# Kernel tuning notes

Measured on AMD Instinct MI355X. Metric: run time of the kernel, lower is better.

The kernel has to match this reference:

```python
import jax, jax.numpy as jnp
import numpy as np

FILTERS = 64
NBITS = 4
NUE = 4
NSPU = 2
NST = NUE * NSPU           # 8 streams total
OUT_CH = NST * NBITS       # 32 output channels
NBS, NANT = 1, 16
CIN = NBS * NANT * 2 + NBS * NANT * NUE * NSPU * 2 + NUE * NSPU + 1  # 297


def hard_sigmoid(x):
    # Keras ConvLSTM2D default recurrent_activation
    return jnp.clip(0.2 * x + 0.5, 0.0, 1.0)


def conv2d(x, w):
    # x: [N,H,W,C], w: [kh,kw,Cin,Cout], SAME padding
    return jax.lax.conv_general_dilated(x, w, (1, 1), 'SAME',
                                        dimension_numbers=('NHWC', 'HWIO', 'NHWC'))


def convlstm2d(x, Wx, Wh, b):
    """Keras ConvLSTM2D (return_sequences=True), gate order i,f,c,o.
    x: [B,T,H,W,Cin] -> [B,T,H,W,F].
    Input-to-hidden convs are precomputed for all timesteps at once;
    only the cheap hidden-to-hidden conv is inside the scan."""
    B, T, H, W, Cin = x.shape
    F = Wh.shape[2]
    xz = conv2d(x.reshape(B * T, H, W, Cin), Wx).reshape(B, T, H, W, 4 * F) + b
    xz = jnp.moveaxis(xz, 1, 0)  # [T,B,H,W,4F]
    h0 = jnp.zeros((B, H, W, F), x.dtype)

    def step(carry, z_in):
        h, c = carry
        z = z_in + conv2d(h, Wh)
        zi, zf, zg, zo = jnp.split(z, 4, axis=-1)
        i = hard_sigmoid(zi)
        f = hard_sigmoid(zf)
        g = jnp.tanh(zg)
        o = hard_sigmoid(zo)
        c = f * c + i * g
        h = o * jnp.tanh(c)
        return (h, c), h

    _, hs = jax.lax.scan(step, (h0, h0), xz)
    return jnp.moveaxis(hs, 0, 1)  # [B,T,H,W,F]


def _lstm_params(key, cin, f, scale=0.05):
    k1, k2, k3 = jax.random.split(key, 3)
    Wx = jax.random.normal(k1, (3, 3, cin, 4 * f), jnp.float32) * scale
    Wh = jax.random.normal(k2, (3, 3, f, 4 * f), jnp.float32) * scale
    b = jax.random.normal(k3, (4 * f,), jnp.float32) * scale
    return Wx, Wh, b


def setup_inputs() -> dict:
    key = jax.random.key(0)
    ks = jax.random.split(key, 10)
    B, T, W = 2, 14, 1536
    inp = {
        'y_ri': jax.random.normal(ks[0], (B, NBS, NANT, T, W, 2), jnp.float32),
        'h_ri': jax.random.normal(ks[1], (B, NBS, NANT, NUE, NSPU, T, W, 2), jnp.float32),
        'err_var': jax.random.uniform(ks[2], (1, 1, 1, NUE, NSPU, T, W), jnp.float32),
        'no': jax.random.uniform(ks[3], (1,), jnp.float32),
    }
    inp['Wx_in'], inp['Wh_in'], inp['b_in'] = _lstm_params(ks[4], CIN, FILTERS)
    inp['Wx_r0'], inp['Wh_r0'], inp['b_r0'] = _lstm_params(ks[5], FILTERS, FILTERS)
    inp['Wx_r1'], inp['Wh_r1'], inp['b_r1'] = _lstm_params(ks[6], FILTERS, FILTERS)
    inp['Wx_out'], inp['Wh_out'], inp['b_out'] = _lstm_params(ks[7], FILTERS, OUT_CH)
    return inp


def _forward(y_ri, h_ri, err_var, no,
             Wx_in, Wh_in, b_in,
             Wx_r0, Wh_r0, b_r0,
             Wx_r1, Wh_r1, b_r1,
             Wx_out, Wh_out, b_out):
    B, nbs, nant, T, W, _ = y_ri.shape
    # y: [B,nbs,nant,T,W,2] -> [B,T,W,nbs*nant*2]
    y_feats = jnp.transpose(y_ri, (0, 3, 4, 1, 2, 5)).reshape(B, T, W, -1)
    # h: [B,nbs,nant,ue,spu,T,W,2] -> [B,T,W,nbs*nant*ue*spu*2]
    h_feats = jnp.transpose(h_ri, (0, 5, 6, 1, 2, 3, 4, 7)).reshape(B, T, W, -1)
    # err_var: [1,1,1,ue,spu,T,W] -> [B,T,W,ue*spu]
    ev = jnp.transpose(err_var[0, 0, 0], (2, 3, 0, 1)).reshape(1, T, W, NUE * NSPU)
    err_feats = jnp.broadcast_to(ev, (B, T, W, NUE * NSPU))
    no_feat = jnp.broadcast_to(no.reshape(1, 1, 1, 1), (B, T, W, 1))
    z = jnp.concatenate([y_feats, h_feats, err_feats, no_feat], axis=-1)
    z = z[:, :, :, None, :]  # [B,T,W,1,C]

    z = convlstm2d(z, Wx_in, Wh_in, b_in)
    # residual blocks (in_ch == filters, so identity skip)
    z = convlstm2d(z, Wx_r0, Wh_r0, b_r0) + z
    z = convlstm2d(z, Wx_r1, Wh_r1, b_r1) + z
    z = convlstm2d(z, Wx_out, Wh_out, b_out)

    z = z[:, :, :, 0, :]  # [B,T,W,OUT_CH]
    N = T * W
    z = z.reshape(B, N, NUE, NSPU, NBITS)
    z = jnp.transpose(z, (0, 2, 3, 1, 4))
    return z.reshape(B, NUE, NSPU, N * NBITS)


def reference(y_ri, h_ri, err_var, no,
              Wx_in, Wh_in, b_in,
              Wx_r0, Wh_r0, b_r0,
              Wx_r1, Wh_r1, b_r1,
              Wx_out, Wh_out, b_out):
    return _forward(y_ri, h_ri, err_var, no,
                    Wx_in, Wh_in, b_in,
                    Wx_r0, Wh_r0, b_r0,
                    Wx_r1, Wh_r1, b_r1,
                    Wx_out, Wh_out, b_out)
```

## Files before the change

### kernel.cpp

```cpp
#include <hip/hip_runtime.h>
#include <hip/hip_bf16.h>


#define BB   2
#define TT   14
#define LL   1536
#define LL2  1538
#define CINR 297
#define CP_IN 320
#define NSTRIP 96
#define NBLK  (BB * NSTRIP)
#define WIN  48

typedef __attribute__((ext_vector_type(8))) short short8;
typedef __attribute__((ext_vector_type(4))) float floatx4;

static constexpr size_t U_WBIN_HI  = 0;
static constexpr size_t U_WBIN_LO  = 245760;
static constexpr size_t U_WBR0_HI  = 491520;
static constexpr size_t U_WBR0_LO  = 540672;
static constexpr size_t U_WBR1_HI  = 589824;
static constexpr size_t U_WBR1_LO  = 638976;
static constexpr size_t U_WBOUT_HI = 688128;
static constexpr size_t U_WBOUT_LO = 712704;
static constexpr size_t U_WHTIN    = 737280;
static constexpr size_t U_WHTR0    = 786432;
static constexpr size_t U_WHTR1    = 835584;
static constexpr size_t U_WHTOUT   = 884736;
static constexpr size_t OFF_BIN   = 448512;
static constexpr size_t OFF_BR0   = 448768;
static constexpr size_t OFF_BR1   = 449024;
static constexpr size_t OFF_BOUT  = 449280;
static constexpr size_t OFF_Z0HI  = 458752;
static constexpr size_t SZ_Z0PL   = 6890240;
static constexpr size_t OFF_Z0LO  = OFF_Z0HI + SZ_Z0PL;
static constexpr size_t OFF_XZ    = OFF_Z0LO + SZ_Z0PL;
static constexpr size_t SZ_XZ     = (size_t)BB*TT*LL*256;
static constexpr size_t OFF_SEQ   = OFF_Z0HI;
static constexpr size_t OFF_SEQHI = OFF_SEQ + (size_t)BB*TT*LL2*64;
static constexpr size_t OFF_SEQLO = OFF_SEQHI + (size_t)BB*TT*LL2*32;

__device__ __forceinline__ float hsig(float x) {
    return fminf(fmaxf(0.2f * x + 0.5f, 0.0f), 1.0f);
}
__device__ __forceinline__ float ftanh(float x) {
    float e = __expf(2.0f * x);
    return 1.0f - 2.0f / (e + 1.0f);
}
__device__ __forceinline__ unsigned short f2bf(float x) {
    unsigned int u = __builtin_bit_cast(unsigned int, x);
    u += 0x7fffu + ((u >> 16) & 1u);
    return (unsigned short)(u >> 16);
}
__device__ __forceinline__ float bf2f(unsigned short h) {
    unsigned int u = ((unsigned int)h) << 16;
    return __builtin_bit_cast(float, u);
}

__global__ __launch_bounds__(256)
void zero_pads_kernel(unsigned short* __restrict__ z0hi,
                      unsigned short* __restrict__ z0lo)
{
    int idx = blockIdx.x * 256 + threadIdx.x;
    const int NZ = BB * TT * 2 * CP_IN;
    if (idx < NZ) {
        int c = idx % CP_IN, r2 = idx / CP_IN;
        int p = r2 >> 1, e = r2 & 1;
        long long off = ((long long)p * LL2 + (e ? (LL2 - 1) : 0)) * CP_IN + c;
        z0hi[off] = 0; z0lo[off] = 0;
    }
}

__global__ __launch_bounds__(256)
void zero_seq_pads_kernel(unsigned short* __restrict__ seqhb,
                          unsigned short* __restrict__ seqlb)
{
    int idx = blockIdx.x * 256 + threadIdx.x;
    const int NS = BB * TT * 2 * 64;
    if (idx < NS) {
        int c = idx % 64, r2 = idx / 64;
        int p = r2 >> 1, e = r2 & 1;
        long long off = ((long long)p * LL2 + (e ? (LL2 - 1) : 0)) * 64 + c;
        seqhb[off] = 0; seqlb[off] = 0;
    }
}

__global__ __launch_bounds__(256)
void prep_weights_kernel(const float* wx_in, const float* wh_in, const float* b_in,
                         const float* wx_r0, const float* wh_r0, const float* b_r0,
                         const float* wx_r1, const float* wh_r1, const float* b_r1,
                         const float* wx_out, const float* wh_out, const float* b_out,
                         float* __restrict__ ws)
{
    int idx = blockIdx.x * 256 + threadIdx.x;
    unsigned short* u = (unsigned short*)ws;
    if (idx < 245760) {
        int j = idx & 7, lane = (idx >> 3) & 63, frag = idx >> 9;
        int g = frag & 15, rest = frag >> 4;
        int kh = rest % 3, cc = rest / 3;
        int mm = lane & 15, quad = lane >> 4;
        int n = g * 16 + mm;
        int ci = cc * 32 + quad * 8 + j;
        float v = 0.0f;
        if (ci < CINR)
            v = wx_in[((size_t)(kh * 3 + 1) * CINR + ci) * 256 + (n & 3) * 64 + (n >> 2)];
        unsigned short hi = f2bf(v);
        u[U_WBIN_HI + idx] = hi;
        u[U_WBIN_LO + idx] = f2bf(v - bf2f(hi));
        return;
    }
    idx -= 245760;
    if (idx < 49152) {
        int j = idx & 7, lane = (idx >> 3) & 63, frag = idx >> 9;
        int g = frag & 15, rest = frag >> 4;
        int kh = rest % 3, cc = rest / 3;
        int mm = lane & 15, quad = lane >> 4;
        int n = g * 16 + mm;
        int ci = cc * 32 + quad * 8 + j;
        float v = wx_r0[((size_t)(kh * 3 + 1) * 64 + ci) * 256 + (n & 3) * 64 + (n >> 2)];
        unsigned short hi = f2bf(v);
        u[U_WBR0_HI + idx] = hi;
        u[U_WBR0_LO + idx] = f2bf(v - bf2f(hi));
        return;
    }
    idx -= 49152;
    if (idx < 49152) {
        int j = idx & 7, lane = (idx >> 3) & 63, frag = idx >> 9;
        int g = frag & 15, rest = frag >> 4;
        int kh = rest % 3, cc = rest / 3;
        int mm = lane & 15, quad = lane >> 4;
        int n = g * 16 + mm;
        int ci = cc * 32 + quad * 8 + j;
        float v = wx_r1[((size_t)(kh * 3 + 1) * 64 + ci) * 256 + (n & 3) * 64 + (n >> 2)];
        unsigned short hi = f2bf(v);
        u[U_WBR1_HI + idx] = hi;
        u[U_WBR1_LO + idx] = f2bf(v - bf2f(hi));
        return;
    }
    idx -= 49152;
    if (idx < 24576) {
        int j = idx & 7, lane = (idx >> 3) & 63, frag = idx >> 9;
        int g = frag & 7, rest = frag >> 3;
        int kh = rest % 3, cc = rest / 3;
        int mm = lane & 15, quad = lane >> 4;
        int n = g * 16 + mm;
        int ci = cc * 32 + quad * 8 + j;
        float v = wx_out[((size_t)(kh * 3 + 1) * 64 + ci) * 128 + (n & 3) * 32 + (n >> 2)];
        unsigned short hi = f2bf(v);
        u[U_WBOUT_HI + idx] = hi;
        u[U_WBOUT_LO + idx] = f2bf(v - bf2f(hi));
        return;
    }
    idx -= 24576;
    if (idx < 49152) {
        int n = idx / 192, k = idx % 192, kh = k >> 6, ci = k & 63;
        u[U_WHTIN + idx] = f2bf(wh_in[((size_t)(kh * 3 + 1) * 64 + ci) * 256 + n]);
        return;
    }
    idx -= 49152;
    if (idx < 49152) {
        int n = idx / 192, k = idx % 192, kh = k >> 6, ci = k & 63;
        u[U_WHTR0 + idx] = f2bf(wh_r0[((size_t)(kh * 3 + 1) * 64 + ci) * 256 + n]);
        return;
    }
    idx -= 49152;
    if (idx < 49152) {
        int n = idx / 192, k = idx % 192, kh = k >> 6, ci = k & 63;
        u[U_WHTR1 + idx] = f2bf(wh_r1[((size_t)(kh * 3 + 1) * 64 + ci) * 256 + n]);
        return;
    }
    idx -= 49152;
    if (idx < 12288) {
        int n = idx / 96, k = idx % 96, kh = k / 32, ci = k % 32;
        u[U_WHTOUT + idx] = f2bf(wh_out[((size_t)(kh * 3 + 1) * 32 + ci) * 128 + n]);
        return;
    }
    idx -= 12288;
    if (idx < 256) { int f = idx >> 2, g = idx & 3; ws[OFF_BIN + idx] = b_in[g * 64 + f]; return; }
    idx -= 256;
    if (idx < 256) { int f = idx >> 2, g = idx & 3; ws[OFF_BR0 + idx] = b_r0[g * 64 + f]; return; }
    idx -= 256;
    if (idx < 256) { int f = idx >> 2, g = idx & 3; ws[OFF_BR1 + idx] = b_r1[g * 64 + f]; return; }
    idx -= 256;
    if (idx < 128) { int f = idx >> 2, g = idx & 3; ws[OFF_BOUT + idx] = b_out[g * 32 + f]; return; }
}

__global__ __launch_bounds__(256)
void build_features_kernel(const float* __restrict__ y,
                           const float* __restrict__ h,
                           const float* __restrict__ ev,
                           const float* __restrict__ no,
                           unsigned short* __restrict__ z0hi,
                           unsigned short* __restrict__ z0lo)
{
    long long idx = (long long)blockIdx.x * 256 + threadIdx.x;
    const long long total = (long long)BB * TT * LL * CP_IN;
    if (idx >= total) return;
    int c = (int)(idx % CP_IN);
    long long rest = idx / CP_IN;
    int l = (int)(rest % LL); rest /= LL;
    int t = (int)(rest % TT);
    int b = (int)(rest / TT);
    float v = 0.0f;
    if (c < 32) {
        int na = c >> 1, ri = c & 1;
        v = y[((((long long)b * 16 + na) * TT + t) * LL + l) * 2 + ri];
    } else if (c < 288) {
        int q = c - 32;
        int ri = q & 1, nspu = (q >> 1) & 1, nue = (q >> 2) & 3, na = q >> 4;
        v = h[((((((long long)b * 16 + na) * 4 + nue) * 2 + nspu) * TT + t) * LL + l) * 2 + ri];
    } else if (c < 296) {
        int q = c - 288; int nspu = q & 1, nue = q >> 1;
        v = ev[(((long long)(nue * 2 + nspu) * TT + t) * LL) + l];
    } else if (c == 296) {
        v = no[0];
    }
    const long long widx = (((long long)(b * TT + t)) * LL2 + (l + 1)) * CP_IN + c;
    unsigned short hi = f2bf(v);
    z0hi[widx] = hi;
    z0lo[widx] = f2bf(v - bf2f(hi));
}

template <int CP>
__global__ __launch_bounds__(256)
void xz_gemm_mfma_kernel(const unsigned short* __restrict__ Ahi,
                         const unsigned short* __restrict__ Alo,
                         const unsigned short* __restrict__ Bphi,
                         const unsigned short* __restrict__ Bplo,
                         const float* __restrict__ bias,
                         float* __restrict__ out, int Ncol)
{
    constexpr int NCm = CP / 64;
    __shared__ unsigned short AsHi[66 * 72], AsLo[66 * 72];
    const int tid  = threadIdx.x;
    const int lane = tid & 63;
    const int wv   = tid >> 6;
    const int m    = lane & 15;
    const int quad = lane >> 4;
    const int bt   = blockIdx.y;
    const int l0   = blockIdx.x * 64;
    const int n0   = blockIdx.z * 128;
    const int NG   = Ncol >> 4;
    const int gBase = (n0 >> 4) + wv;

    const int r0s = tid >> 3,        c0 = (tid & 7) * 8;
    const int r1s = (tid + 256) >> 3, c1 = (tid & 7) * 8;
    const int r2s = 64 + (tid >> 3),  c2 = (tid & 7) * 8;
    const long long aG0 = ((long long)bt * LL2 + l0 + r0s) * CP + c0;
    const long long aG1 = ((long long)bt * LL2 + l0 + r1s) * CP + c1;
    const long long aG2 = ((long long)bt * LL2 + l0 + r2s) * CP + c2;

    short8 g0h, g0l, g1h, g1l, g2h = (short8)0, g2l = (short8)0;

    g0h = *reinterpret_cast<const short8*>(&Ahi[aG0]);
    g0l = *reinterpret_cast<const short8*>(&Alo[aG0]);
    g1h = *reinterpret_cast<const short8*>(&Ahi[aG1]);
    g1l = *reinterpret_cast<const short8*>(&Alo[aG1]);
    if (tid < 16) {
        g2h = *reinterpret_cast<const short8*>(&Ahi[aG2]);
        g2l = *reinterpret_cast<const short8*>(&Alo[aG2]);
    }

    floatx4 acc[4][2];
#pragma unroll
    for (int i = 0; i < 4; i++)
#pragma unroll
        for (int j = 0; j < 2; j++) acc[i][j] = (floatx4){0.f, 0.f, 0.f, 0.f};

#pragma unroll 1
    for (int mc = 0; mc < NCm; ++mc) {
        __syncthreads();
        *reinterpret_cast<short8*>(&AsHi[r0s * 72 + c0]) = g0h;
        *reinterpret_cast<short8*>(&AsLo[r0s * 72 + c0]) = g0l;
        *reinterpret_cast<short8*>(&AsHi[r1s * 72 + c1]) = g1h;
        *reinterpret_cast<short8*>(&AsLo[r1s * 72 + c1]) = g1l;
        if (tid < 16) {
            *reinterpret_cast<short8*>(&AsHi[r2s * 72 + c2]) = g2h;
            *reinterpret_cast<short8*>(&AsLo[r2s * 72 + c2]) = g2l;
        }
        __syncthreads();
        if (mc + 1 < NCm) {
            const int co = (mc + 1) * 64;
            g0h = *reinterpret_cast<const short8*>(&Ahi[aG0 + co]);
            g0l = *reinterpret_cast<const short8*>(&Alo[aG0 + co]);
            g1h = *reinterpret_cast<const short8*>(&Ahi[aG1 + co]);
            g1l = *reinterpret_cast<const short8*>(&Alo[aG1 + co]);
            if (tid < 16) {
                g2h = *reinterpret_cast<const short8*>(&Ahi[aG2 + co]);
                g2l = *reinterpret_cast<const short8*>(&Alo[aG2 + co]);
            }
        }
#pragma unroll
        for (int sub = 0; sub < 2; ++sub) {
            const int cc = mc * 2 + sub;
            short8 bh[3][2], bl[3][2];
#pragma unroll
            for (int kh = 0; kh < 3; ++kh)
#pragma unroll
                for (int nt = 0; nt < 2; ++nt) {
                    const size_t off =
                        ((size_t)((cc * 3 + kh) * NG + gBase + nt * 4)) * 512 + lane * 8;
                    bh[kh][nt] = *reinterpret_cast<const short8*>(&Bphi[off]);
                    bl[kh][nt] = *reinterpret_cast<const short8*>(&Bplo[off]);
                }
#pragma unroll
            for (int kh = 0; kh < 3; ++kh) {
#pragma unroll
                for (int mt = 0; mt < 4; ++mt) {
                    const int aofs = (mt * 16 + m + kh) * 72 + sub * 32 + quad * 8;
                    const short8 ah = *reinterpret_cast<const short8*>(&AsHi[aofs]);
                    const short8 al = *reinterpret_cast<const short8*>(&AsLo[aofs]);
                    acc[mt][0] = __builtin_amdgcn_mfma_f32_16x16x32_bf16(al, bh[kh][0], acc[mt][0], 0, 0, 0);
                    acc[mt][0] = __builtin_amdgcn_mfma_f32_16x16x32_bf16(ah, bl[kh][0], acc[mt][0], 0, 0, 0);
                    acc[mt][0] = __builtin_amdgcn_mfma_f32_16x16x32_bf16(ah, bh[kh][0], acc[mt][0], 0, 0, 0);
                    acc[mt][1] = __builtin_amdgcn_mfma_f32_16x16x32_bf16(al, bh[kh][1], acc[mt][1], 0, 0, 0);
                    acc[mt][1] = __builtin_amdgcn_mfma_f32_16x16x32_bf16(ah, bl[kh][1], acc[mt][1], 0, 0, 0);
                    acc[mt][1] = __builtin_amdgcn_mfma_f32_16x16x32_bf16(ah, bh[kh][1], acc[mt][1], 0, 0, 0);
                }
            }
        }
    }

#pragma unroll
    for (int nt = 0; nt < 2; ++nt) {
        const int col = n0 + nt * 64 + wv * 16 + m;
        const float bv = bias[col];
#pragma unroll
        for (int mt = 0; mt < 4; ++mt) {
#pragma unroll
            for (int reg = 0; reg < 4; ++reg) {
                int l = l0 + mt * 16 + quad * 4 + reg;
                out[((size_t)bt * LL + l) * Ncol + col] = acc[mt][nt][reg] + bv;
            }
        }
    }
}

template <int F_, bool RESID, bool OUTW>
__global__ __launch_bounds__(64 * (F_ / 16))
void lstm_scan_kernel(const float* __restrict__ xz,
                      const unsigned short* __restrict__ WhT,
                      float* seq,
                      unsigned short* __restrict__ seqhb,
                      unsigned short* __restrict__ seqlb,
                      float* __restrict__ dout)
{
    constexpr int NW = F_ / 16;
    constexpr int NT = 64 * NW;
    constexpr int K  = 3 * F_;
    constexpr int KS = K / 32;
    constexpr int KH = KS / 3;
    constexpr int HP = F_ + 8;
    __shared__ unsigned short Hs[2][(WIN + 2) * HP];

    const int tid  = threadIdx.x;
    const int lane = tid & 63;
    const int wv   = tid >> 6;
    const int m    = lane & 15;
    const int quad = lane >> 4;
    const int blk  = blockIdx.x;
    const int b    = blk / NSTRIP;
    const int o0   = (blk % NSTRIP) * 16;
    const int f    = wv * 16 + m;

    short8 bfr[4][KS];
#pragma unroll
    for (int g = 0; g < 4; g++)
#pragma unroll
        for (int ks = 0; ks < KS; ks++) {
            const int n  = g * F_ + f;
            const int k0 = ks * 32 + quad * 8;
            bfr[g][ks] = *reinterpret_cast<const short8*>(&WhT[(size_t)n * K + k0]);
        }

    for (int idx = tid; idx < (WIN + 2) * HP; idx += NT) {
        Hs[0][idx] = 0; Hs[1][idx] = 0;
    }
    __syncthreads();

    float c[3][4];
#pragma unroll
    for (int i = 0; i < 3; i++)
#pragma unroll
        for (int j = 0; j < 4; j++) c[i][j] = 0.0f;

    int cur = 0;
    for (int t = 0; t < TT; ++t) {
        const size_t btL  = ((size_t)b * TT + t) * LL;
        const size_t btLP = ((size_t)b * TT + t) * LL2;

        float4 xzv[3][4];
        float  rsv[4];
#pragma unroll
        for (int mt = 0; mt < 3; ++mt)
#pragma unroll
            for (int reg = 0; reg < 4; ++reg) {
                const int w = mt * 16 + quad * 4 + reg;
                const int l = o0 - 16 + w;
                float4 v = make_float4(0.f, 0.f, 0.f, 0.f);
                if (l >= 0 && l < LL && w >= t && w < WIN - t)
                    v = *reinterpret_cast<const float4*>(
                        &xz[(btL + l) * (size_t)(4 * F_) + f * 4]);
                xzv[mt][reg] = v;
            }
        if (RESID) {
#pragma unroll
            for (int reg = 0; reg < 4; ++reg) {
                const int l = o0 + quad * 4 + reg;
                rsv[reg] = seq[(btLP + 1 + l) * F_ + f];
            }
        }

        const int nxt = cur ^ 1;
#pragma unroll
        for (int mt = 0; mt < 3; ++mt) {
            floatx4 zi = {0.f, 0.f, 0.f, 0.f};
            floatx4 zf = {0.f, 0.f, 0.f, 0.f};
            floatx4 zg = {0.f, 0.f, 0.f, 0.f};
            floatx4 zo = {0.f, 0.f, 0.f, 0.f};
            if (t > 0) {
#pragma unroll
                for (int kh = 0; kh < 3; kh++) {
#pragma unroll
                    for (int hf = 0; hf < KH; hf++) {
                        const short8 af = *reinterpret_cast<const short8*>(
                            &Hs[cur][(mt * 16 + m + kh) * HP + hf * 32 + quad * 8]);
                        const int ks = kh * KH + hf;
                        zi = __builtin_amdgcn_mfma_f32_16x16x32_bf16(af, bfr[0][ks], zi, 0, 0, 0);
                        zf = __builtin_amdgcn_mfma_f32_16x16x32_bf16(af, bfr[1][ks], zf, 0, 0, 0);
                        zg = __builtin_amdgcn_mfma_f32_16x16x32_bf16(af, bfr[2][ks], zg, 0, 0, 0);
                        zo = __builtin_amdgcn_mfma_f32_16x16x32_bf16(af, bfr[3][ks], zo, 0, 0, 0);
                    }
                }
            }
#pragma unroll
            for (int reg = 0; reg < 4; ++reg) {
                const int w = mt * 16 + quad * 4 + reg;
                const int l = o0 - 16 + w;
                const bool valid = (l >= 0 && l < LL);
                const float4 z4 = xzv[mt][reg];
                const float ig = hsig(z4.x + zi[reg]);
                const float fg = hsig(z4.y + zf[reg]);
                const float gg = ftanh(z4.z + zg[reg]);
                const float og = hsig(z4.w + zo[reg]);
                float cn = fg * c[mt][reg] + ig * gg;
                float hn = og * ftanh(cn);
                if (!valid) { cn = 0.0f; hn = 0.0f; }
                c[mt][reg] = cn;
                Hs[nxt][(1 + w) * HP + f] = f2bf(hn);
                if (w >= 16 && w < 32) {
                    if (OUTW) {
                        const int ue = f >> 3, spu = (f >> 2) & 1, bit = f & 3;
                        const size_t n = (size_t)t * LL + l;
                        dout[(((size_t)b * 4 + ue) * 2 + spu) * ((size_t)TT * LL * 4)
                             + n * 4 + bit] = hn;
                    } else {
                        float v = hn;
                        if (RESID) v += rsv[reg];
                        seq[(btLP + 1 + l) * F_ + f] = v;
                        const unsigned short hi = f2bf(v);
                        seqhb[(btLP + 1 + l) * F_ + f] = hi;
                        seqlb[(btLP + 1 + l) * F_ + f] = f2bf(v - bf2f(hi));
                    }
                }
            }
        }
        __syncthreads();
        cur = nxt;
    }
}

extern "C" void kernel_launch(void* const* d_in, const int* in_sizes, int n_in,
                              void* d_out, int out_size, void* d_ws, size_t ws_size,
                              hipStream_t stream)
{
    (void)in_sizes; (void)n_in; (void)out_size; (void)ws_size;
    const float* y_ri   = (const float*)d_in[0];
    const float* h_ri   = (const float*)d_in[1];
    const float* evar   = (const float*)d_in[2];
    const float* no     = (const float*)d_in[3];
    const float* wx_in  = (const float*)d_in[4];
    const float* wh_in  = (const float*)d_in[5];
    const float* b_in   = (const float*)d_in[6];
    const float* wx_r0  = (const float*)d_in[7];
    const float* wh_r0  = (const float*)d_in[8];
    const float* b_r0   = (const float*)d_in[9];
    const float* wx_r1  = (const float*)d_in[10];
    const float* wh_r1  = (const float*)d_in[11];
    const float* b_r1   = (const float*)d_in[12];
    const float* wx_out = (const float*)d_in[13];
    const float* wh_out = (const float*)d_in[14];
    const float* b_out  = (const float*)d_in[15];

    float* ws = (float*)d_ws;
    unsigned short* wu = (unsigned short*)d_ws;
    float* dout = (float*)d_out;

    unsigned short* z0hi = (unsigned short*)(ws + OFF_Z0HI);
    unsigned short* z0lo = (unsigned short*)(ws + OFF_Z0LO);
    float* xz    = ws + OFF_XZ;
    float* seq   = ws + OFF_SEQ;
    unsigned short* seqhb = (unsigned short*)(ws + OFF_SEQHI);
    unsigned short* seqlb = (unsigned short*)(ws + OFF_SEQLO);

    zero_pads_kernel<<<70, 256, 0, stream>>>(z0hi, z0lo);
    prep_weights_kernel<<<2068, 256, 0, stream>>>(
        wx_in, wh_in, b_in, wx_r0, wh_r0, b_r0,
        wx_r1, wh_r1, b_r1, wx_out, wh_out, b_out, ws);
    {
        long long total = (long long)BB * TT * LL * CP_IN;
        int blocks = (int)((total + 255) / 256);
        build_features_kernel<<<blocks, 256, 0, stream>>>(
            y_ri, h_ri, evar, no, z0hi, z0lo);
    }

    const dim3 gIn(LL / 64, BB * TT, 2);
    const dim3 gO (LL / 64, BB * TT, 1);

    xz_gemm_mfma_kernel<CP_IN><<<gIn, 256, 0, stream>>>(
        z0hi, z0lo, wu + U_WBIN_HI, wu + U_WBIN_LO, ws + OFF_BIN, xz, 256);
    zero_seq_pads_kernel<<<14, 256, 0, stream>>>(seqhb, seqlb);
    lstm_scan_kernel<64, false, false><<<NBLK, 256, 0, stream>>>(
        xz, wu + U_WHTIN, seq, seqhb, seqlb, nullptr);

    xz_gemm_mfma_kernel<64><<<gIn, 256, 0, stream>>>(
        seqhb, seqlb, wu + U_WBR0_HI, wu + U_WBR0_LO, ws + OFF_BR0, xz, 256);
    lstm_scan_kernel<64, true, false><<<NBLK, 256, 0, stream>>>(
        xz, wu + U_WHTR0, seq, seqhb, seqlb, nullptr);

    xz_gemm_mfma_kernel<64><<<gIn, 256, 0, stream>>>(
        seqhb, seqlb, wu + U_WBR1_HI, wu + U_WBR1_LO, ws + OFF_BR1, xz, 256);
    lstm_scan_kernel<64, true, false><<<NBLK, 256, 0, stream>>>(
        xz, wu + U_WHTR1, seq, seqhb, seqlb, nullptr);

    xz_gemm_mfma_kernel<64><<<gO, 256, 0, stream>>>(
        seqhb, seqlb, wu + U_WBOUT_HI, wu + U_WBOUT_LO, ws + OFF_BOUT, xz, 128);
    lstm_scan_kernel<32, false, true><<<NBLK, 128, 0, stream>>>(
        xz, wu + U_WHTOUT, nullptr, nullptr, nullptr, dout);
}
```

Baseline: 482.3 us.

## Prefetch next timestep xz into registers and shrink owned strip to 12

Restructures the recurrent scan so the next timestep's input-projection and residual loads are issued before the current step's MFMA work, using ping-pong register buffers and a two-step unrolled loop. This hides global load latency behind compute. It also changes the strip ownership from 16 to 12 output columns per block, centered at offset 18 in the 48-wide window, which raises the block count from 96 to 128 strips per batch. The cost is more register pressure from the double-buffered xz values and more redundant halo recomputation per useful output.

```diff
diff --git a/kernel.cpp b/kernel.cpp
--- a/kernel.cpp
+++ b/kernel.cpp
@@ -8,7 +8,9 @@
 #define LL2  1538
 #define CINR 297
 #define CP_IN 320
-#define NSTRIP 96
+#define NSTRIP 128
+#define OWN    12
+#define OWN0   18
 #define NBLK  (BB * NSTRIP)
 #define WIN  48
 
@@ -360,7 +362,7 @@
     const int quad = lane >> 4;
     const int blk  = blockIdx.x;
     const int b    = blk / NSTRIP;
-    const int o0   = (blk % NSTRIP) * 16;
+    const int o0   = (blk % NSTRIP) * OWN;
     const int f    = wv * 16 + m;
 
     short8 bfr[4][KS];
@@ -384,90 +386,132 @@
 #pragma unroll
         for (int j = 0; j < 4; j++) c[i][j] = 0.0f;
 
-    int cur = 0;
-    for (int t = 0; t < TT; ++t) {
-        const size_t btL  = ((size_t)b * TT + t) * LL;
-        const size_t btLP = ((size_t)b * TT + t) * LL2;
-
-        float4 xzv[3][4];
-        float  rsv[4];
+    float4 xzA[3][4], xzB[3][4];
+    float  rsA[4] = {0.f, 0.f, 0.f, 0.f}, rsB[4] = {0.f, 0.f, 0.f, 0.f};
+
+    {
+        const size_t btLn = (size_t)b * TT * LL;
 #pragma unroll
         for (int mt = 0; mt < 3; ++mt)
 #pragma unroll
             for (int reg = 0; reg < 4; ++reg) {
                 const int w = mt * 16 + quad * 4 + reg;
-                const int l = o0 - 16 + w;
+                const int l = o0 - OWN0 + w;
                 float4 v = make_float4(0.f, 0.f, 0.f, 0.f);
-                if (l >= 0 && l < LL && w >= t && w < WIN - t)
+                if (l >= 0 && l < LL)
                     v = *reinterpret_cast<const float4*>(
-                        &xz[(btL + l) * (size_t)(4 * F_) + f * 4]);
-                xzv[mt][reg] = v;
+                        &xz[(btLn + l) * (size_t)(4 * F_) + f * 4]);
+                xzA[mt][reg] = v;
             }
         if (RESID) {
+            const size_t btLPn = (size_t)b * TT * LL2;
 #pragma unroll
             for (int reg = 0; reg < 4; ++reg) {
-                const int l = o0 + quad * 4 + reg;
-                rsv[reg] = seq[(btLP + 1 + l) * F_ + f];
+                const int w = 16 + quad * 4 + reg;
+                float v = 0.f;
+                if (w >= OWN0 && w < OWN0 + OWN)
+                    v = seq[(btLPn + 1 + o0 + (w - OWN0)) * F_ + f];
+                rsA[reg] = v;
             }
         }
-
-        const int nxt = cur ^ 1;
-#pragma unroll
-        for (int mt = 0; mt < 3; ++mt) {
-            floatx4 zi = {0.f, 0.f, 0.f, 0.f};
-            floatx4 zf = {0.f, 0.f, 0.f, 0.f};
-            floatx4 zg = {0.f, 0.f, 0.f, 0.f};
-            floatx4 zo = {0.f, 0.f, 0.f, 0.f};
-            if (t > 0) {
-#pragma unroll
-                for (int kh = 0; kh < 3; kh++) {
-#pragma unroll
-                    for (int hf = 0; hf < KH; hf++) {
-                        const short8 af = *reinterpret_cast<const short8*>(
-                            &Hs[cur][(mt * 16 + m + kh) * HP + hf * 32 + quad * 8]);
-                        const int ks = kh * KH + hf;
-                        zi = __builtin_amdgcn_mfma_f32_16x16x32_bf16(af, bfr[0][ks], zi, 0, 0, 0);
-                        zf = __builtin_amdgcn_mfma_f32_16x16x32_bf16(af, bfr[1][ks], zf, 0, 0, 0);
-                        zg = __builtin_amdgcn_mfma_f32_16x16x32_bf16(af, bfr[2][ks], zg, 0, 0, 0);
-                        zo = __builtin_amdgcn_mfma_f32_16x16x32_bf16(af, bfr[3][ks], zo, 0, 0, 0);
-                    }
-                }
-            }
-#pragma unroll
-            for (int reg = 0; reg < 4; ++reg) {
-                const int w = mt * 16 + quad * 4 + reg;
-                const int l = o0 - 16 + w;
-                const bool valid = (l >= 0 && l < LL);
-                const float4 z4 = xzv[mt][reg];
-                const float ig = hsig(z4.x + zi[reg]);
-                const float fg = hsig(z4.y + zf[reg]);
-                const float gg = ftanh(z4.z + zg[reg]);
-                const float og = hsig(z4.w + zo[reg]);
-                float cn = fg * c[mt][reg] + ig * gg;
-                float hn = og * ftanh(cn);
-                if (!valid) { cn = 0.0f; hn = 0.0f; }
-                c[mt][reg] = cn;
-                Hs[nxt][(1 + w) * HP + f] = f2bf(hn);
-                if (w >= 16 && w < 32) {
-                    if (OUTW) {
-                        const int ue = f >> 3, spu = (f >> 2) & 1, bit = f & 3;
-                        const size_t n = (size_t)t * LL + l;
-                        dout[(((size_t)b * 4 + ue) * 2 + spu) * ((size_t)TT * LL * 4)
-                             + n * 4 + bit] = hn;
-                    } else {
-                        float v = hn;
-                        if (RESID) v += rsv[reg];
-                        seq[(btLP + 1 + l) * F_ + f] = v;
-                        const unsigned short hi = f2bf(v);
-                        seqhb[(btLP + 1 + l) * F_ + f] = hi;
-                        seqlb[(btLP + 1 + l) * F_ + f] = f2bf(v - bf2f(hi));
-                    }
-                }
-            }
-        }
-        __syncthreads();
-        cur = nxt;
-    }
+    }
+
+    int cur = 0;
+
+#define SCAN_STEP(T, XZC, RSC, XZN, RSN)                                       \
+    {                                                                          \
+        const int t = (T);                                                     \
+        if (t + 1 < TT) {                                                      \
+            const size_t btLn = ((size_t)b * TT + (t + 1)) * LL;               \
+            _Pragma("unroll")                                                  \
+            for (int mt = 0; mt < 3; ++mt)                                     \
+                _Pragma("unroll")                                              \
+                for (int reg = 0; reg < 4; ++reg) {                            \
+                    const int w = mt * 16 + quad * 4 + reg;                    \
+                    const int l = o0 - OWN0 + w;                               \
+                    float4 v = make_float4(0.f, 0.f, 0.f, 0.f);                \
+                    if (l >= 0 && l < LL && w >= t + 1 && w < WIN - (t + 1))   \
+                        v = *reinterpret_cast<const float4*>(                  \
+                            &xz[(btLn + l) * (size_t)(4 * F_) + f * 4]);       \
+                    XZN[mt][reg] = v;                                          \
+                }                                                              \
+            if (RESID) {                                                       \
+                const size_t btLPn = ((size_t)b * TT + (t + 1)) * LL2;         \
+                _Pragma("unroll")                                              \
+                for (int reg = 0; reg < 4; ++reg) {                            \
+                    const int w = 16 + quad * 4 + reg;                         \
+                    float v = 0.f;                                             \
+                    if (w >= OWN0 && w < OWN0 + OWN)                           \
+                        v = seq[(btLPn + 1 + o0 + (w - OWN0)) * F_ + f];       \
+                    RSN[reg] = v;                                              \
+                }                                                              \
+            }                                                                  \
+        }                                                                      \
+        const size_t btLP = ((size_t)b * TT + t) * LL2;                        \
+        const int nxt = cur ^ 1;                                               \
+        _Pragma("unroll")                                                      \
+        for (int mt = 0; mt < 3; ++mt) {                                       \
+            floatx4 zi = {0.f, 0.f, 0.f, 0.f};                                 \
+            floatx4 zf = {0.f, 0.f, 0.f, 0.f};                                 \
+            floatx4 zg = {0.f, 0.f, 0.f, 0.f};                                 \
+            floatx4 zo = {0.f, 0.f, 0.f, 0.f};                                 \
+            if (t > 0) {                                                       \
+                _Pragma("unroll")                                              \
+                for (int kh = 0; kh < 3; kh++) {                               \
+                    _Pragma("unroll")                                          \
+                    for (int hf = 0; hf < KH; hf++) {                          \
+                        const short8 af = *reinterpret_cast<const short8*>(    \
+                            &Hs[cur][(mt * 16 + m + kh) * HP + hf * 32 + quad * 8]); \
+                        const int ks = kh * KH + hf;                           \
+                        zi = __builtin_amdgcn_mfma_f32_16x16x32_bf16(af, bfr[0][ks], zi, 0, 0, 0); \
+                        zf = __builtin_amdgcn_mfma_f32_16x16x32_bf16(af, bfr[1][ks], zf, 0, 0, 0); \
+                        zg = __builtin_amdgcn_mfma_f32_16x16x32_bf16(af, bfr[2][ks], zg, 0, 0, 0); \
+                        zo = __builtin_amdgcn_mfma_f32_16x16x32_bf16(af, bfr[3][ks], zo, 0, 0, 0); \
+                    }                                                          \
+                }                                                              \
+            }                                                                  \
+            _Pragma("unroll")                                                  \
+            for (int reg = 0; reg < 4; ++reg) {                                \
+                const int w = mt * 16 + quad * 4 + reg;                        \
+                const int l = o0 - OWN0 + w;                                   \
+                const bool valid = (l >= 0 && l < LL);                         \
+                const float4 z4 = XZC[mt][reg];                                \
+                const float ig = hsig(z4.x + zi[reg]);                         \
+                const float fg = hsig(z4.y + zf[reg]);                         \
+                const float gg = ftanh(z4.z + zg[reg]);                        \
+                const float og = hsig(z4.w + zo[reg]);                         \
+                float cn = fg * c[mt][reg] + ig * gg;                          \
+                float hn = og * ftanh(cn);                                     \
+                if (!valid) { cn = 0.0f; hn = 0.0f; }                          \
+                c[mt][reg] = cn;                                               \
+                Hs[nxt][(1 + w) * HP + f] = f2bf(hn);                          \
+                if (w >= OWN0 && w < OWN0 + OWN) {                             \
+                    if (OUTW) {                                                \
+                        const int ue = f >> 3, spu = (f >> 2) & 1, bit = f & 3;\
+                        const size_t n = (size_t)t * LL + l;                   \
+                        dout[(((size_t)b * 4 + ue) * 2 + spu) * ((size_t)TT * LL * 4) \
+                             + n * 4 + bit] = hn;                              \
+                    } else {                                                   \
+                        float v = hn;                                          \
+                        if (RESID) v += RSC[reg];                              \
+                        seq[(btLP + 1 + l) * F_ + f] = v;                      \
+                        const unsigned short hi2 = f2bf(v);                    \
+                        seqhb[(btLP + 1 + l) * F_ + f] = hi2;                  \
+                        seqlb[(btLP + 1 + l) * F_ + f] = f2bf(v - bf2f(hi2));  \
+                    }                                                          \
+                }                                                              \
+            }                                                                  \
+        }                                                                      \
+        __syncthreads();                         \
+        cur = nxt;                                                             \
+    }
+
+#pragma unroll 1
+    for (int t2 = 0; t2 < TT; t2 += 2) {
+        SCAN_STEP(t2,     xzA, rsA, xzB, rsB)
+        SCAN_STEP(t2 + 1, xzB, rsB, xzA, rsA)
+    }
+#undef SCAN_STEP
 }
 
 extern "C" void kernel_launch(void* const* d_in, const int* in_sizes, int n_in,
```

After: 505.4 us. +4.8%, slower.

## Split LSTM scan row tiles across waves and shrink owned strip width

Applied to the files above, without the earlier changes.

The recurrent scan kernel now gives each of the three 16-row tiles of the 48-wide halo window its own wavefront, so blocks run 3x as many threads and each wave does one tile's MFMAs instead of looping over three. Each block's owned output width drops from 16 to 12 columns (centered with an 18-column halo), raising the strip count from 96 to 128 and the total block count. This increases parallelism and cuts per-wave serial work per timestep. The cost is more redundant halo computation and weight register loads duplicated across waves.

```diff
diff --git a/kernel.cpp b/kernel.cpp
--- a/kernel.cpp
+++ b/kernel.cpp
@@ -8,7 +8,9 @@
 #define LL2  1538
 #define CINR 297
 #define CP_IN 320
-#define NSTRIP 96
+#define NSTRIP 128
+#define OWN    12
+#define OWN0   18
 #define NBLK  (BB * NSTRIP)
 #define WIN  48
 
@@ -337,7 +339,7 @@
 }
 
 template <int F_, bool RESID, bool OUTW>
-__global__ __launch_bounds__(64 * (F_ / 16))
+__global__ __launch_bounds__(192 * (F_ / 16), (F_ == 64) ? 3 : 2)
 void lstm_scan_kernel(const float* __restrict__ xz,
                       const unsigned short* __restrict__ WhT,
                       float* seq,
@@ -345,123 +347,115 @@
                       unsigned short* __restrict__ seqlb,
                       float* __restrict__ dout)
 {
-    constexpr int NW = F_ / 16;
-    constexpr int NT = 64 * NW;
-    constexpr int K  = 3 * F_;
-    constexpr int KS = K / 32;
-    constexpr int KH = KS / 3;
-    constexpr int HP = F_ + 8;
+    constexpr int NWF = F_ / 16;
+    constexpr int NT  = 192 * NWF;
+    constexpr int K   = 3 * F_;
+    constexpr int KS  = K / 32;
+    constexpr int KH  = KS / 3;
+    constexpr int HP  = F_ + 8;
     __shared__ unsigned short Hs[2][(WIN + 2) * HP];
 
     const int tid  = threadIdx.x;
     const int lane = tid & 63;
-    const int wv   = tid >> 6;
+    const int wid  = tid >> 6;
+    const int mt   = wid / NWF;
+    const int fg   = wid - mt * NWF;
     const int m    = lane & 15;
     const int quad = lane >> 4;
-    const int blk  = blockIdx.x;
-    const int b    = blk / NSTRIP;
-    const int o0   = (blk % NSTRIP) * 16;
-    const int f    = wv * 16 + m;
+    const int b    = blockIdx.x / NSTRIP;
+    const int o0   = (blockIdx.x % NSTRIP) * OWN;
+    const int f    = fg * 16 + m;
 
     short8 bfr[4][KS];
 #pragma unroll
     for (int g = 0; g < 4; g++)
 #pragma unroll
-        for (int ks = 0; ks < KS; ks++) {
-            const int n  = g * F_ + f;
-            const int k0 = ks * 32 + quad * 8;
-            bfr[g][ks] = *reinterpret_cast<const short8*>(&WhT[(size_t)n * K + k0]);
-        }
+        for (int ks = 0; ks < KS; ks++)
+            bfr[g][ks] = *reinterpret_cast<const short8*>(
+                &WhT[(size_t)(g * F_ + f) * K + ks * 32 + quad * 8]);
 
     for (int idx = tid; idx < (WIN + 2) * HP; idx += NT) {
         Hs[0][idx] = 0; Hs[1][idx] = 0;
     }
     __syncthreads();
 
-    float c[3][4];
-#pragma unroll
-    for (int i = 0; i < 3; i++)
-#pragma unroll
-        for (int j = 0; j < 4; j++) c[i][j] = 0.0f;
+    float c[4];
+#pragma unroll
+    for (int j = 0; j < 4; j++) c[j] = 0.0f;
 
     int cur = 0;
+#pragma unroll 1
     for (int t = 0; t < TT; ++t) {
         const size_t btL  = ((size_t)b * TT + t) * LL;
         const size_t btLP = ((size_t)b * TT + t) * LL2;
 
-        float4 xzv[3][4];
+        float4 xzv[4];
         float  rsv[4];
 #pragma unroll
-        for (int mt = 0; mt < 3; ++mt)
-#pragma unroll
-            for (int reg = 0; reg < 4; ++reg) {
-                const int w = mt * 16 + quad * 4 + reg;
-                const int l = o0 - 16 + w;
-                float4 v = make_float4(0.f, 0.f, 0.f, 0.f);
-                if (l >= 0 && l < LL && w >= t && w < WIN - t)
-                    v = *reinterpret_cast<const float4*>(
-                        &xz[(btL + l) * (size_t)(4 * F_) + f * 4]);
-                xzv[mt][reg] = v;
+        for (int reg = 0; reg < 4; ++reg) {
+            const int w = mt * 16 + quad * 4 + reg;
+            const int l = o0 - OWN0 + w;
+            float4 v = make_float4(0.f, 0.f, 0.f, 0.f);
+            if (l >= 0 && l < LL && w >= t && w < WIN - t)
+                v = *reinterpret_cast<const float4*>(
+                    &xz[(btL + l) * (size_t)(4 * F_) + f * 4]);
+            xzv[reg] = v;
+            if (RESID) {
+                float rv = 0.f;
+                if (w >= OWN0 && w < OWN0 + OWN)
+                    rv = seq[(btLP + 1 + l) * F_ + f];
+                rsv[reg] = rv;
             }
-        if (RESID) {
-#pragma unroll
-            for (int reg = 0; reg < 4; ++reg) {
-                const int l = o0 + quad * 4 + reg;
-                rsv[reg] = seq[(btLP + 1 + l) * F_ + f];
-            }
-        }
-
-        const int nxt = cur ^ 1;
-#pragma unroll
-        for (int mt = 0; mt < 3; ++mt) {
-            floatx4 zi = {0.f, 0.f, 0.f, 0.f};
-            floatx4 zf = {0.f, 0.f, 0.f, 0.f};
-            floatx4 zg = {0.f, 0.f, 0.f, 0.f};
-            floatx4 zo = {0.f, 0.f, 0.f, 0.f};
-            if (t > 0) {
-#pragma unroll
-                for (int kh = 0; kh < 3; kh++) {
-#pragma unroll
-                    for (int hf = 0; hf < KH; hf++) {
-                        const short8 af = *reinterpret_cast<const short8*>(
-                            &Hs[cur][(mt * 16 + m + kh) * HP + hf * 32 + quad * 8]);
-                        const int ks = kh * KH + hf;
-                        zi = __builtin_amdgcn_mfma_f32_16x16x32_bf16(af, bfr[0][ks], zi, 0, 0, 0);
-                        zf = __builtin_amdgcn_mfma_f32_16x16x32_bf16(af, bfr[1][ks], zf, 0, 0, 0);
-                        zg = __builtin_amdgcn_mfma_f32_16x16x32_bf16(af, bfr[2][ks], zg, 0, 0, 0);
-                        zo = __builtin_amdgcn_mfma_f32_16x16x32_bf16(af, bfr[3][ks], zo, 0, 0, 0);
-                    }
+        }
+
+        floatx4 zi = {0.f, 0.f, 0.f, 0.f};
+        floatx4 zf = {0.f, 0.f, 0.f, 0.f};
+        floatx4 zg = {0.f, 0.f, 0.f, 0.f};
+        floatx4 zo = {0.f, 0.f, 0.f, 0.f};
+        if (t > 0) {
+#pragma unroll
+            for (int kh = 0; kh < 3; kh++) {
+#pragma unroll
+                for (int hf = 0; hf < KH; hf++) {
+                    const short8 af = *reinterpret_cast<const short8*>(
+                        &Hs[cur][(mt * 16 + m + kh) * HP + hf * 32 + quad * 8]);
+                    const int ks = kh * KH + hf;
+                    zi = __builtin_amdgcn_mfma_f32_16x16x32_bf16(af, bfr[0][ks], zi, 0, 0, 0);
+                    zf = __builtin_amdgcn_mfma_f32_16x16x32_bf16(af, bfr[1][ks], zf, 0, 0, 0);
+                    zg = __builtin_amdgcn_mfma_f32_16x16x32_bf16(af, bfr[2][ks], zg, 0, 0, 0);
+                    zo = __builtin_amdgcn_mfma_f32_16x16x32_bf16(af, bfr[3][ks], zo, 0, 0, 0);
                 }
             }
-#pragma unroll
-            for (int reg = 0; reg < 4; ++reg) {
-                const int w = mt * 16 + quad * 4 + reg;
-                const int l = o0 - 16 + w;
-                const bool valid = (l >= 0 && l < LL);
-                const float4 z4 = xzv[mt][reg];
-                const float ig = hsig(z4.x + zi[reg]);
-                const float fg = hsig(z4.y + zf[reg]);
-                const float gg = ftanh(z4.z + zg[reg]);
-                const float og = hsig(z4.w + zo[reg]);
-                float cn = fg * c[mt][reg] + ig * gg;
-                float hn = og * ftanh(cn);
-                if (!valid) { cn = 0.0f; hn = 0.0f; }
-                c[mt][reg] = cn;
-                Hs[nxt][(1 + w) * HP + f] = f2bf(hn);
-                if (w >= 16 && w < 32) {
-                    if (OUTW) {
-                        const int ue = f >> 3, spu = (f >> 2) & 1, bit = f & 3;
-                        const size_t n = (size_t)t * LL + l;
-                        dout[(((size_t)b * 4 + ue) * 2 + spu) * ((size_t)TT * LL * 4)
-                             + n * 4 + bit] = hn;
-                    } else {
-                        float v = hn;
-                        if (RESID) v += rsv[reg];
-                        seq[(btLP + 1 + l) * F_ + f] = v;
-                        const unsigned short hi = f2bf(v);
-                        seqhb[(btLP + 1 + l) * F_ + f] = hi;
-                        seqlb[(btLP + 1 + l) * F_ + f] = f2bf(v - bf2f(hi));
-                    }
+        }
+        const int nxt = cur ^ 1;
+#pragma unroll
+        for (int reg = 0; reg < 4; ++reg) {
+            const int w = mt * 16 + quad * 4 + reg;
+            const int l = o0 - OWN0 + w;
+            const bool valid = (l >= 0 && l < LL);
+            const float4 z4 = xzv[reg];
+            const float ig  = hsig(z4.x + zi[reg]);
+            const float fgt = hsig(z4.y + zf[reg]);
+            const float gg  = ftanh(z4.z + zg[reg]);
+            const float og  = hsig(z4.w + zo[reg]);
+            float cn = fgt * c[reg] + ig * gg;
+            float hn = og * ftanh(cn);
+            if (!valid) { cn = 0.0f; hn = 0.0f; }
+            c[reg] = cn;
+            Hs[nxt][(1 + w) * HP + f] = f2bf(hn);
+            if (w >= OWN0 && w < OWN0 + OWN) {
+                if (OUTW) {
+                    const int ue = f >> 3, spu = (f >> 2) & 1, bit = f & 3;
+                    const size_t n = (size_t)t * LL + l;
+                    dout[(((size_t)b * 4 + ue) * 2 + spu) * ((size_t)TT * LL * 4)
+                         + n * 4 + bit] = hn;
+                } else {
+                    float v = hn;
+                    if (RESID) v += rsv[reg];
+                    seq[(btLP + 1 + l) * F_ + f] = v;
+                    const unsigned short hi2 = f2bf(v);
+                    seqhb[(btLP + 1 + l) * F_ + f] = hi2;
+                    seqlb[(btLP + 1 + l) * F_ + f] = f2bf(v - bf2f(hi2));
                 }
             }
         }
@@ -520,21 +514,21 @@
     xz_gemm_mfma_kernel<CP_IN><<<gIn, 256, 0, stream>>>(
         z0hi, z0lo, wu + U_WBIN_HI, wu + U_WBIN_LO, ws + OFF_BIN, xz, 256);
     zero_seq_pads_kernel<<<14, 256, 0, stream>>>(seqhb, seqlb);
-    lstm_scan_kernel<64, false, false><<<NBLK, 256, 0, stream>>>(
+    lstm_scan_kernel<64, false, false><<<NBLK, 768, 0, stream>>>(
         xz, wu + U_WHTIN, seq, seqhb, seqlb, nullptr);
 
     xz_gemm_mfma_kernel<64><<<gIn, 256, 0, stream>>>(
         seqhb, seqlb, wu + U_WBR0_HI, wu + U_WBR0_LO, ws + OFF_BR0, xz, 256);
-    lstm_scan_kernel<64, true, false><<<NBLK, 256, 0, stream>>>(
+    lstm_scan_kernel<64, true, false><<<NBLK, 768, 0, stream>>>(
         xz, wu + U_WHTR0, seq, seqhb, seqlb, nullptr);
 
     xz_gemm_mfma_kernel<64><<<gIn, 256, 0, stream>>>(
         seqhb, seqlb, wu + U_WBR1_HI, wu + U_WBR1_LO, ws + OFF_BR1, xz, 256);
-    lstm_scan_kernel<64, true, false><<<NBLK, 256, 0, stream>>>(
+    lstm_scan_kernel<64, true, false><<<NBLK, 768, 0, stream>>>(
         xz, wu + U_WHTR1, seq, seqhb, seqlb, nullptr);
 
     xz_gemm_mfma_kernel<64><<<gO, 256, 0, stream>>>(
         seqhb, seqlb, wu + U_WBOUT_HI, wu + U_WBOUT_LO, ws + OFF_BOUT, xz, 128);
-    lstm_scan_kernel<32, false, true><<<NBLK, 128, 0, stream>>>(
+    lstm_scan_kernel<32, false, true><<<NBLK, 384, 0, stream>>>(
         xz, wu + U_WHTOUT, nullptr, nullptr, nullptr, dout);
 }
```

Measured after the change: 501.9 us. 4.1% more time.
